# Kernel optimization log

Measured on AMD Instinct MI355X. Metric: run time of the kernel, lower is better.

## Reference

```python
import jax, jax.numpy as jnp
import numpy as np

NEG_SLOPE = 0.2
LN_EPS = 1e-5
NUM_LAYERS = 4
H = 3            # num heads (both modalities)
C_MOL = 512      # molecule channels (in == out, required by the cat in forward)
C_PROT = 1280    # protein channels
VOCAB = 512 * 9 + 1
G_MOL = 512      # molecule graphs
G_PROT = 32      # protein graphs


def _with_self_loops(src, dst, n):
    loop = jnp.arange(n, dtype=src.dtype)
    return jnp.concatenate([src, loop]), jnp.concatenate([dst, loop])


def gat_conv(x, src, dst, W, a_src, a_dst, bias):
    """PyG GATConv, concat=False (head-mean), add_self_loops=True.
    x: [N, Fin], W: [Fin, H*C], a_src/a_dst: [H, C], bias: [C]."""
    n = x.shape[0]
    h = (x @ W).reshape(n, a_src.shape[0], a_src.shape[1])   # [N,H,C]
    al_s = jnp.sum(h * a_src, axis=-1)                       # [N,H]
    al_d = jnp.sum(h * a_dst, axis=-1)                       # [N,H]
    s, d = _with_self_loops(src, dst, n)
    e = jax.nn.leaky_relu(al_s[s] + al_d[d], NEG_SLOPE)      # [E+N,H]
    m = jax.ops.segment_max(e, d, num_segments=n)            # segment softmax (stable)
    m = jnp.where(jnp.isfinite(m), m, 0.0)
    p = jnp.exp(e - m[d])
    z = jax.ops.segment_sum(p, d, num_segments=n)
    alpha = p / (z[d] + 1e-16)                               # [E+N,H]
    out = jax.ops.segment_sum(h[s] * alpha[:, :, None], d, num_segments=n)  # [N,H,C]
    return out.mean(axis=1) + bias                           # concat=False -> head mean


def layer_norm(x, g, b):
    mu = x.mean(-1, keepdims=True)
    var = ((x - mu) ** 2).mean(-1, keepdims=True)
    return (x - mu) * jax.lax.rsqrt(var + LN_EPS) * g + b


def mean_pool(x, batch, num_graphs):
    s = jax.ops.segment_sum(x, batch, num_segments=num_graphs)
    cnt = jax.ops.segment_sum(jnp.ones((x.shape[0],), x.dtype), batch, num_segments=num_graphs)
    return s / jnp.maximum(cnt, 1.0)[:, None]


def setup_inputs() -> dict:
    key = jax.random.key(0)
    ks = jax.random.split(key, 20)
    n_mol, e_mol = 40000, 80000
    n_prot, e_prot = 8000, 64000
    drug_x = jax.random.randint(ks[0], (n_mol, 9), 0, VOCAB)
    mol_edge_index = jax.random.randint(ks[1], (2, e_mol), 0, n_mol)
    mol_batch = jnp.sort(jax.random.randint(ks[2], (n_mol,), 0, G_MOL))
    prot_x = jax.random.normal(ks[3], (n_prot, C_PROT), jnp.float32)
    prot_edge_index = jax.random.randint(ks[4], (2, e_prot), 0, n_prot)
    prot_batch = jnp.sort(jax.random.randint(ks[5], (n_prot,), 0, G_PROT))
    sc = 0.02
    emb = (jax.random.normal(ks[6], (VOCAB, C_MOL), jnp.float32) * sc).at[0].set(0.0)  # padding_idx=0
    mol_W = jax.random.normal(ks[7], (NUM_LAYERS, C_MOL, H * C_MOL), jnp.float32) * sc
    mol_asrc = jax.random.normal(ks[8], (NUM_LAYERS, H, C_MOL), jnp.float32) * sc
    mol_adst = jax.random.normal(ks[9], (NUM_LAYERS, H, C_MOL), jnp.float32) * sc
    mol_bias = jnp.zeros((NUM_LAYERS, C_MOL), jnp.float32)
    mol_ln_g = jnp.ones((NUM_LAYERS, C_MOL), jnp.float32)
    mol_ln_b = jnp.zeros((NUM_LAYERS, C_MOL), jnp.float32)
    prot_W = jax.random.normal(ks[10], (NUM_LAYERS, C_PROT, H * C_PROT), jnp.float32) * sc
    prot_asrc = jax.random.normal(ks[11], (NUM_LAYERS, H, C_PROT), jnp.float32) * sc
    prot_adst = jax.random.normal(ks[12], (NUM_LAYERS, H, C_PROT), jnp.float32) * sc
    prot_bias = jnp.zeros((NUM_LAYERS, C_PROT), jnp.float32)
    prot_ln_g = jnp.ones((NUM_LAYERS, C_PROT), jnp.float32)
    prot_ln_b = jnp.zeros((NUM_LAYERS, C_PROT), jnp.float32)
    return dict(drug_x=drug_x, mol_edge_index=mol_edge_index, mol_batch=mol_batch,
                prot_x=prot_x, prot_edge_index=prot_edge_index, prot_batch=prot_batch,
                emb=emb, mol_W=mol_W, mol_asrc=mol_asrc, mol_adst=mol_adst,
                mol_bias=mol_bias, mol_ln_g=mol_ln_g, mol_ln_b=mol_ln_b,
                prot_W=prot_W, prot_asrc=prot_asrc, prot_adst=prot_adst,
                prot_bias=prot_bias, prot_ln_g=prot_ln_g, prot_ln_b=prot_ln_b)


def reference(drug_x, mol_edge_index, mol_batch, prot_x, prot_edge_index, prot_batch,
              emb, mol_W, mol_asrc, mol_adst, mol_bias, mol_ln_g, mol_ln_b,
              prot_W, prot_asrc, prot_adst, prot_bias, prot_ln_g, prot_ln_b):
    # dropout layers are identity (eval mode)
    mol_x = emb[drug_x].mean(axis=-2)                       # [N_mol, C_MOL]
    mol_feats = [mean_pool(mol_x, mol_batch, G_MOL)]
    prot_feats = [mean_pool(prot_x, prot_batch, G_PROT)]
    msrc, mdst = mol_edge_index[0], mol_edge_index[1]
    psrc, pdst = prot_edge_index[0], prot_edge_index[1]
    px = prot_x
    for i in range(NUM_LAYERS):
        mol_x = gat_conv(mol_x, msrc, mdst, mol_W[i], mol_asrc[i], mol_adst[i], mol_bias[i])
        mol_x = layer_norm(mol_x, mol_ln_g[i], mol_ln_b[i])
        px = gat_conv(px, psrc, pdst, prot_W[i], prot_asrc[i], prot_adst[i], prot_bias[i])
        px = layer_norm(px, prot_ln_g[i], prot_ln_b[i])
        mol_feats.append(mean_pool(mol_x, mol_batch, G_MOL))
        prot_feats.append(mean_pool(px, prot_batch, G_PROT))
    return jnp.stack(mol_feats, axis=1), jnp.stack(prot_feats, axis=1)  # [G,5,C] each
```

## Files before the change

### kernel.cpp

```cpp
#include <hip/hip_runtime.h>
#include <cstdint>


constexpr int H_HEADS = 3;
constexpr float NEG_SLOPE = 0.2f;
constexpr float LN_EPS = 1e-5f;
constexpr int N_MOL = 40000, E_MOL = 80000, C_MOL = 512, G_MOL = 512;
constexpr int N_PROT = 8000, E_PROT = 64000, C_PROT = 1280, G_PROT = 32;
constexpr int LAYERS = 4;
constexpr int MPAD_MOL = 40064;
constexpr int MPAD_PROT = 8064;

typedef unsigned short u16;
typedef __attribute__((ext_vector_type(8))) short short8v;
typedef __attribute__((ext_vector_type(4))) unsigned short ushort4v;
typedef __attribute__((ext_vector_type(4))) float f32x4;

__device__ __forceinline__ float bf2f(u16 s) {
    union { unsigned u; float f; } v; v.u = ((unsigned)s) << 16; return v.f;
}
__device__ __forceinline__ u16 f2bf(float f) {
    union { float f; unsigned u; } v; v.f = f;
    return (u16)((v.u + 0x7fffu + ((v.u >> 16) & 1u)) >> 16);
}

__device__ __forceinline__ void g2l16(const void* g, void* l) {
    __builtin_amdgcn_global_load_lds((const __attribute__((address_space(1))) void*)g,
                                     (__attribute__((address_space(3))) void*)l, 16, 0, 0);
}


__global__ void set_int_kernel(int* p, int v, int n) {
    int i = blockIdx.x * blockDim.x + threadIdx.x;
    if (i < n) p[i] = v;
}

__global__ void zero_f32_kernel(float* p, int n) {
    int i = blockIdx.x * blockDim.x + threadIdx.x;
    if (i < n) p[i] = 0.f;
}

__global__ void copy_int_kernel(const int* __restrict__ s, int* __restrict__ d, int n) {
    int i = blockIdx.x * blockDim.x + threadIdx.x;
    if (i < n) d[i] = s[i];
}

__global__ void hist_kernel(const int* __restrict__ keys, int n, int* __restrict__ cnt) {
    int i = blockIdx.x * blockDim.x + threadIdx.x;
    if (i < n) atomicAdd(&cnt[keys[i]], 1);
}

__global__ void scan_kernel(const int* __restrict__ in, int* __restrict__ out, int n) {
    __shared__ int sums[1024];
    const int t = threadIdx.x;
    const int chunk = (n + 1023) / 1024;
    const int start = t * chunk;
    const int end = min(start + chunk, n);
    int s = 0;
    for (int i = start; i < end; ++i) s += in[i];
    sums[t] = s;
    __syncthreads();
    if (t == 0) {
        int acc = 0;
        for (int i = 0; i < 1024; ++i) { int v = sums[i]; sums[i] = acc; acc += v; }
        out[n] = acc;
    }
    __syncthreads();
    int acc = sums[t];
    for (int i = start; i < end; ++i) { out[i] = acc; acc += in[i]; }
}

__global__ void fill_self_kernel(int* __restrict__ pos, int* __restrict__ srcl, int n) {
    int i = blockIdx.x * blockDim.x + threadIdx.x;
    if (i < n) { int slot = atomicAdd(&pos[i], 1); srcl[slot] = i; }
}

__global__ void fill_edge_kernel(const int* __restrict__ src, const int* __restrict__ dst, int e,
                                 int* __restrict__ pos, int* __restrict__ srcl) {
    int i = blockIdx.x * blockDim.x + threadIdx.x;
    if (i < e) { int slot = atomicAdd(&pos[dst[i]], 1); srcl[slot] = src[i]; }
}

__global__ void f32_to_bf16(const float* __restrict__ in, u16* __restrict__ out, int n) {
    int i = blockIdx.x * blockDim.x + threadIdx.x;
    if (i < n) out[i] = f2bf(in[i]);
}


__global__ void embed_mean_kernel(const int* __restrict__ drug_x, const float* __restrict__ emb,
                                  u16* __restrict__ out) {
    const int n = blockIdx.x;
    __shared__ int idx[9];
    if (threadIdx.x < 9) idx[threadIdx.x] = drug_x[n * 9 + threadIdx.x];
    __syncthreads();
    const int c = threadIdx.x;
    float s = 0.f;
#pragma unroll
    for (int t = 0; t < 9; ++t) s += emb[(size_t)idx[t] * C_MOL + c];
    out[(size_t)n * C_MOL + c] = f2bf(s * (1.f / 9.f));
}


__global__ __launch_bounds__(256) void transfold(const float* __restrict__ W, u16* __restrict__ Wt,
                                                 const float* __restrict__ asrc,
                                                 const float* __restrict__ adst,
                                                 float* __restrict__ wsrc, float* __restrict__ wdst,
                                                 int CIN, int COUT, size_t headStride, int ldn) {
    __shared__ float t[32][33];
    __shared__ float rs[8][33], rd[8][33];
    const int h = blockIdx.z;
    const int n0 = blockIdx.x * 32, k0 = blockIdx.y * 32;
    const int tx = threadIdx.x & 31, ty = threadIdx.x >> 5;
#pragma unroll
    for (int q = 0; q < 4; ++q)
        t[ty + q * 8][tx] = W[(size_t)(k0 + ty + q * 8) * (H_HEADS * COUT) + h * COUT + n0 + tx];
    __syncthreads();
#pragma unroll
    for (int q = 0; q < 4; ++q)
        Wt[(size_t)h * headStride + (size_t)(n0 + ty + q * 8) * ldn + k0 + tx] =
            f2bf(t[tx][ty + q * 8]);
    float ps = 0.f, pd = 0.f;
    const float* as = asrc + h * COUT + n0;
    const float* ad = adst + h * COUT + n0;
#pragma unroll
    for (int q = 0; q < 4; ++q) {
        const float w = t[tx][ty + q * 8];
        ps += w * as[ty + q * 8];
        pd += w * ad[ty + q * 8];
    }
    rs[ty][tx] = ps;
    rd[ty][tx] = pd;
    __syncthreads();
    if (ty == 0) {
        float s = 0.f, d = 0.f;
#pragma unroll
        for (int j = 0; j < 8; ++j) { s += rs[j][tx]; d += rd[j][tx]; }
        atomicAdd(&wsrc[h * CIN + k0 + tx], s);
        atomicAdd(&wdst[h * CIN + k0 + tx], d);
    }
}


template <int C>
__global__ void attn_logits(const u16* __restrict__ x, const float* __restrict__ wsrc,
                            const float* __restrict__ wdst, float* __restrict__ als,
                            float* __restrict__ ald) {
    constexpr int PER = C / 64;
    const int n = blockIdx.x, lane = threadIdx.x;
    const u16* xr = x + (size_t)n * C + lane * PER;
    float xv[PER];
#pragma unroll
    for (int i = 0; i < PER; i += 4) {
        const ushort4v v = *(const ushort4v*)(xr + i);
        xv[i] = bf2f(v.x); xv[i + 1] = bf2f(v.y); xv[i + 2] = bf2f(v.z); xv[i + 3] = bf2f(v.w);
    }
    for (int h = 0; h < H_HEADS; ++h) {
        const float* ws = wsrc + h * C + lane * PER;
        const float* wd = wdst + h * C + lane * PER;
        float ss = 0.f, sd = 0.f;
#pragma unroll
        for (int i = 0; i < PER; i += 4) {
            const float4 a = *(const float4*)(ws + i);
            const float4 b = *(const float4*)(wd + i);
            ss += xv[i] * a.x + xv[i + 1] * a.y + xv[i + 2] * a.z + xv[i + 3] * a.w;
            sd += xv[i] * b.x + xv[i + 1] * b.y + xv[i + 2] * b.z + xv[i + 3] * b.w;
        }
        for (int o = 32; o; o >>= 1) { ss += __shfl_down(ss, o); sd += __shfl_down(sd, o); }
        if (lane == 0) { als[n * H_HEADS + h] = ss; ald[n * H_HEADS + h] = sd; }
    }
}


__global__ void alpha_kernel2(const float* __restrict__ als, const float* __restrict__ ald,
                              const int* __restrict__ indptr, const int* __restrict__ srcl,
                              float* __restrict__ alphaw, int n_nodes) {
    const int t = blockIdx.x * blockDim.x + threadIdx.x;
    const int n = t / H_HEADS, h = t - n * H_HEADS;
    if (n >= n_nodes) return;
    const int beg = indptr[n], end = indptr[n + 1];
    const float ad = ald[n * H_HEADS + h];
    float m = -1e30f;
    for (int e = beg; e < end; ++e) {
        float v = als[srcl[e] * H_HEADS + h] + ad;
        v = v >= 0.f ? v : NEG_SLOPE * v;
        m = fmaxf(m, v);
    }
    float z = 0.f;
    for (int e = beg; e < end; ++e) {
        float v = als[srcl[e] * H_HEADS + h] + ad;
        v = v >= 0.f ? v : NEG_SLOPE * v;
        z += __expf(v - m);
    }
    const float zi = 1.f / (z + 1e-16f);
    for (int e = beg; e < end; ++e) {
        float v = als[srcl[e] * H_HEADS + h] + ad;
        v = v >= 0.f ? v : NEG_SLOPE * v;
        alphaw[e * H_HEADS + h] = __expf(v - m) * zi;
    }
}


__global__ __launch_bounds__(256) void aggregate_mol(const u16* __restrict__ x,
                                                     const float* __restrict__ alphaw,
                                                     const int* __restrict__ indptr,
                                                     const int* __restrict__ srcl,
                                                     u16* __restrict__ agg) {
    const int wv = threadIdx.x >> 6, lane = threadIdx.x & 63;
    const int n = blockIdx.x * 4 + wv;
    const int beg = indptr[n], end = indptr[n + 1];
    float acc[H_HEADS][8];
#pragma unroll
    for (int h = 0; h < H_HEADS; ++h)
#pragma unroll
        for (int j = 0; j < 8; ++j) acc[h][j] = 0.f;
    for (int e = beg; e < end; ++e) {
        const float a0 = alphaw[e * H_HEADS + 0];
        const float a1 = alphaw[e * H_HEADS + 1];
        const float a2 = alphaw[e * H_HEADS + 2];
        const short8v row = *(const short8v*)(x + (size_t)srcl[e] * C_MOL + lane * 8);
#pragma unroll
        for (int j = 0; j < 8; ++j) {
            const float f = bf2f((u16)row[j]);
            acc[0][j] += a0 * f; acc[1][j] += a1 * f; acc[2][j] += a2 * f;
        }
    }
    u16* o = agg + (size_t)n * (3 * C_MOL) + lane * 8;
#pragma unroll
    for (int h = 0; h < H_HEADS; ++h) {
        short8v r;
#pragma unroll
        for (int j = 0; j < 8; ++j) r[j] = (short)f2bf(acc[h][j]);
        *(short8v*)(o + h * C_MOL) = r;
    }
}


template <int C>
__global__ void aggregate_all3(const u16* __restrict__ x, const float* __restrict__ alphaw,
                               const int* __restrict__ indptr, const int* __restrict__ srcl,
                               u16* __restrict__ agg) {
    const int n = blockIdx.x, tid = threadIdx.x;
    const int beg = indptr[n], end = indptr[n + 1];
    float acc[H_HEADS][4];
#pragma unroll
    for (int h = 0; h < H_HEADS; ++h)
#pragma unroll
        for (int j = 0; j < 4; ++j) acc[h][j] = 0.f;
    for (int e = beg; e < end; ++e) {
        const float a0 = alphaw[e * H_HEADS + 0];
        const float a1 = alphaw[e * H_HEADS + 1];
        const float a2 = alphaw[e * H_HEADS + 2];
        const ushort4v v = *(const ushort4v*)(x + (size_t)srcl[e] * C + tid * 4);
        const float f0 = bf2f(v.x), f1 = bf2f(v.y), f2 = bf2f(v.z), f3 = bf2f(v.w);
        acc[0][0] += a0 * f0; acc[0][1] += a0 * f1; acc[0][2] += a0 * f2; acc[0][3] += a0 * f3;
        acc[1][0] += a1 * f0; acc[1][1] += a1 * f1; acc[1][2] += a1 * f2; acc[1][3] += a1 * f3;
        acc[2][0] += a2 * f0; acc[2][1] += a2 * f1; acc[2][2] += a2 * f2; acc[2][3] += a2 * f3;
    }
    u16* o = agg + (size_t)n * (3 * C) + tid * 4;
#pragma unroll
    for (int h = 0; h < H_HEADS; ++h) {
        ushort4v r;
        r.x = f2bf(acc[h][0]); r.y = f2bf(acc[h][1]); r.z = f2bf(acc[h][2]); r.w = f2bf(acc[h][3]);
        *(ushort4v*)(o + h * C) = r;
    }
}


__global__ __launch_bounds__(512) void gemm_dual(
    const u16* __restrict__ A0, const u16* __restrict__ B0, u16* __restrict__ C0,
    int N0, int K0, int nx0, int M0, int g0,
    const u16* __restrict__ A1, const u16* __restrict__ B1, u16* __restrict__ C1,
    int N1, int K1, int nx1, int M1) {
    __shared__ u16 lds[49152];
    const int tid = threadIdx.x;
    const int w = tid >> 6, l = tid & 63;
    const int wr = w >> 2, wc = w & 3;

    const int bid = blockIdx.x;
    const u16 *A, *Bt;
    u16* Cout;
    int N, K, nxch, Mreal, base, sz;
    if (bid < g0) { base = 0; sz = g0; A = A0; Bt = B0; Cout = C0; N = N0; K = K0; nxch = nx0; Mreal = M0; }
    else { base = g0; sz = gridDim.x - g0; A = A1; Bt = B1; Cout = C1; N = N1; K = K1; nxch = nx1; Mreal = M1; }
    const int j = bid - base;
    const int q = sz >> 3, r = sz & 7;
    const int xcd = j & 7, idx = j >> 3;
    const int wg = (xcd < r ? xcd * (q + 1) : r * (q + 1) + (xcd - r) * q) + idx;
    const int nx = wg % nxch, my = wg / nxch;
    const size_t bm = (size_t)my * 128, bn = (size_t)nx * 256;

    const f32x4 zf = {0.f, 0.f, 0.f, 0.f};
    f32x4 acc[4][4];
#pragma unroll
    for (int i = 0; i < 4; ++i)
#pragma unroll
        for (int jj = 0; jj < 4; ++jj) acc[i][jj] = zf;

    const int sseg = (l & 7) ^ (l >> 3);
    const u16* Ab = A + (bm + w * 16 + (l >> 3)) * (size_t)K + sseg * 8;
    const u16* Bb = Bt + (bn + w * 32 + (l >> 3)) * (size_t)K + sseg * 8;

    auto stage = [&](int buf, int k0) {
        u16* La = lds + buf * 24576;
#pragma unroll
        for (int qq = 0; qq < 2; ++qq)
            g2l16(Ab + k0 + (size_t)qq * 8 * K, La + (w * 2 + qq) * 512);
#pragma unroll
        for (int qq = 0; qq < 4; ++qq)
            g2l16(Bb + k0 + (size_t)qq * 8 * K, La + 8192 + (w * 4 + qq) * 512);
    };

    const int nt = K >> 6;
    stage(0, 0);
    for (int t = 0; t < nt; ++t) {
        const int cur = t & 1;
        if (t + 1 < nt) {
            stage(cur ^ 1, (t + 1) << 6);
            asm volatile("s_waitcnt vmcnt(6)" ::: "memory");
        } else {
            asm volatile("s_waitcnt vmcnt(0)" ::: "memory");
        }
        __builtin_amdgcn_s_barrier();
        __builtin_amdgcn_sched_barrier(0);
        const u16* Lb = lds + cur * 24576;
#pragma unroll
        for (int kk = 0; kk < 2; ++kk) {
            const int gs = kk * 4 + (l >> 4);
            const int sg = (gs ^ (l & 7)) * 8;
            short8v af[4], bf8[4];
#pragma unroll
            for (int fm = 0; fm < 4; ++fm) {
                const int row = wr * 64 + fm * 16 + (l & 15);
                af[fm] = *(const short8v*)&Lb[row * 64 + sg];
            }
#pragma unroll
            for (int fn = 0; fn < 4; ++fn) {
                const int row = wc * 64 + fn * 16 + (l & 15);
                bf8[fn] = *(const short8v*)&Lb[8192 + row * 64 + sg];
            }
#pragma unroll
            for (int fm = 0; fm < 4; ++fm)
#pragma unroll
                for (int fn = 0; fn < 4; ++fn)
                    acc[fm][fn] = __builtin_amdgcn_mfma_f32_16x16x32_bf16(af[fm], bf8[fn],
                                                                          acc[fm][fn], 0, 0, 0);
        }
        __builtin_amdgcn_sched_barrier(0);
        __builtin_amdgcn_s_barrier();
    }

#pragma unroll
    for (int half = 0; half < 2; ++half) {
        if (wr == half) {
#pragma unroll
            for (int fm = 0; fm < 4; ++fm)
#pragma unroll
                for (int fn = 0; fn < 4; ++fn) {
                    const int col = wc * 64 + fn * 16 + (l & 15);
#pragma unroll
                    for (int rr = 0; rr < 4; ++rr)
                        lds[(fm * 16 + (l >> 4) * 4 + rr) * 264 + col] = f2bf(acc[fm][fn][rr]);
                }
        }
        __syncthreads();
        const int lrow = tid >> 3, lseg = tid & 7;
        const size_t grow = bm + half * 64 + lrow;
        if (grow < (size_t)Mreal) {
            u16* Crow = Cout + grow * (size_t)N + bn + lseg * 32;
            const u16* Lr = lds + lrow * 264 + lseg * 32;
#pragma unroll
            for (int ii = 0; ii < 4; ++ii)
                *(float4*)(Crow + ii * 8) = *(const float4*)(Lr + ii * 8);
        }
        __syncthreads();
    }
}


template <int C, int LOGITS>
__global__ __launch_bounds__(256) void ln_kernel(u16* __restrict__ x,
                                                 const float* __restrict__ bias,
                                                 const float* __restrict__ g,
                                                 const float* __restrict__ b,
                                                 const float* __restrict__ wsrc_n,
                                                 const float* __restrict__ wdst_n,
                                                 float* __restrict__ als, float* __restrict__ ald) {
    constexpr int PER = C / 256;
    const int n = blockIdx.x, tid = threadIdx.x;
    u16* xr = x + (size_t)n * C;
    float vals[PER];
    float s1 = 0.f, s2 = 0.f;
    constexpr float invH = 1.f / (float)H_HEADS;
#pragma unroll
    for (int i = 0; i < PER; ++i) {
        const int c = i * 256 + tid;
        const float v = bf2f(xr[c]) * invH + bias[c];
        vals[i] = v;
        s1 += v;
        s2 += v * v;
    }
    __shared__ float red[2][4];
    __shared__ float red2[4][6];
    for (int o = 32; o; o >>= 1) { s1 += __shfl_down(s1, o); s2 += __shfl_down(s2, o); }
    if ((tid & 63) == 0) { red[0][tid >> 6] = s1; red[1][tid >> 6] = s2; }
    __syncthreads();
    const float t1 = red[0][0] + red[0][1] + red[0][2] + red[0][3];
    const float t2 = red[1][0] + red[1][1] + red[1][2] + red[1][3];
    const float mu = t1 / C;
    const float var = t2 / C - mu * mu;
    const float rstd = rsqrtf(var + LN_EPS);
    float ps0 = 0.f, ps1 = 0.f, ps2 = 0.f, pd0 = 0.f, pd1 = 0.f, pd2 = 0.f;
#pragma unroll
    for (int i = 0; i < PER; ++i) {
        const int c = i * 256 + tid;
        const u16 xq16 = f2bf((vals[i] - mu) * rstd * g[c] + b[c]);
        xr[c] = xq16;
        if (LOGITS) {
            const float xq = bf2f(xq16);
            ps0 += xq * wsrc_n[0 * C + c]; pd0 += xq * wdst_n[0 * C + c];
            ps1 += xq * wsrc_n[1 * C + c]; pd1 += xq * wdst_n[1 * C + c];
            ps2 += xq * wsrc_n[2 * C + c]; pd2 += xq * wdst_n[2 * C + c];
        }
    }
    if (LOGITS) {
        for (int o = 32; o; o >>= 1) {
            ps0 += __shfl_down(ps0, o); ps1 += __shfl_down(ps1, o); ps2 += __shfl_down(ps2, o);
            pd0 += __shfl_down(pd0, o); pd1 += __shfl_down(pd1, o); pd2 += __shfl_down(pd2, o);
        }
        __syncthreads();
        if ((tid & 63) == 0) {
            const int wv = tid >> 6;
            red2[wv][0] = ps0; red2[wv][1] = ps1; red2[wv][2] = ps2;
            red2[wv][3] = pd0; red2[wv][4] = pd1; red2[wv][5] = pd2;
        }
        __syncthreads();
        if (tid == 0) {
#pragma unroll
            for (int h = 0; h < H_HEADS; ++h) {
                als[n * H_HEADS + h] = red2[0][h] + red2[1][h] + red2[2][h] + red2[3][h];
                ald[n * H_HEADS + h] =
                    red2[0][3 + h] + red2[1][3 + h] + red2[2][3 + h] + red2[3][3 + h];
            }
        }
    }
}


template <int C, int S>
__global__ void pool_atomic(const u16* __restrict__ x, const int* __restrict__ goff,
                            float* __restrict__ out, int layer) {
    const int g = blockIdx.x, seg = blockIdx.y;
    const int beg = goff[g], end = goff[g + 1];
    const int len = end - beg;
    const int s0 = beg + (len * seg) / S;
    const int s1 = beg + (len * (seg + 1)) / S;
    if (s0 >= s1) return;
    const float inv = 1.f / fmaxf((float)len, 1.f);
    const int tid = threadIdx.x;
    float a0 = 0.f, a1 = 0.f, a2 = 0.f, a3 = 0.f;
    for (int n = s0; n < s1; ++n) {
        const ushort4v v = *(const ushort4v*)(x + (size_t)n * C + tid * 4);
        a0 += bf2f(v.x); a1 += bf2f(v.y); a2 += bf2f(v.z); a3 += bf2f(v.w);
    }
    float* o = out + ((size_t)g * (LAYERS + 1) + layer) * C + tid * 4;
    atomicAdd(o + 0, a0 * inv);
    atomicAdd(o + 1, a1 * inv);
    atomicAdd(o + 2, a2 * inv);
    atomicAdd(o + 3, a3 * inv);
}


extern "C" void kernel_launch(void* const* d_in, const int* in_sizes, int n_in, void* d_out,
                              int out_size, void* d_ws, size_t ws_size, hipStream_t stream) {
    const int* drug_x      = (const int*)d_in[0];
    const int* mol_ei      = (const int*)d_in[1];
    const int* mol_batch   = (const int*)d_in[2];
    const float* prot_in   = (const float*)d_in[3];
    const int* prot_ei     = (const int*)d_in[4];
    const int* prot_batch  = (const int*)d_in[5];
    const float* emb       = (const float*)d_in[6];
    const float* mol_W     = (const float*)d_in[7];
    const float* mol_asrc  = (const float*)d_in[8];
    const float* mol_adst  = (const float*)d_in[9];
    const float* mol_bias  = (const float*)d_in[10];
    const float* mol_lng   = (const float*)d_in[11];
    const float* mol_lnb   = (const float*)d_in[12];
    const float* prot_W    = (const float*)d_in[13];
    const float* prot_asrc = (const float*)d_in[14];
    const float* prot_adst = (const float*)d_in[15];
    const float* prot_bias = (const float*)d_in[16];
    const float* prot_lng  = (const float*)d_in[17];
    const float* prot_lnb  = (const float*)d_in[18];

    if (ws_size < (size_t)240500000) return;
    const bool BIG = ws_size >= (size_t)262000000;

    char* base = (char*)d_ws;
    size_t off = 0;
    auto alloc = [&](size_t bytes) -> void* {
        void* r = base + off;
        off = (off + bytes + 255) & ~(size_t)255;
        return r;
    };
    u16* x_mol  = (u16*)alloc((size_t)N_MOL * C_MOL * 2);
    u16* x_prot = (u16*)alloc((size_t)N_PROT * C_PROT * 2);
    u16* aggM   = (u16*)alloc((size_t)3 * MPAD_MOL * C_MOL * 2);
    u16* WtM    = (u16*)alloc((size_t)H_HEADS * C_MOL * C_MOL * 2);
    u16* WtP    = (u16*)alloc((size_t)H_HEADS * C_PROT * C_PROT * 2);
    u16* aggP   = BIG ? (u16*)alloc((size_t)3 * MPAD_PROT * C_PROT * 2) : aggM;
    float* wsrcM = (float*)alloc((size_t)LAYERS * H_HEADS * C_MOL * 4);
    float* wdstM = (float*)alloc((size_t)LAYERS * H_HEADS * C_MOL * 4);
    float* wsrcP = (float*)alloc((size_t)LAYERS * H_HEADS * C_PROT * 4);
    float* wdstP = (float*)alloc((size_t)LAYERS * H_HEADS * C_PROT * 4);
    float* alsM = (float*)alloc((size_t)N_MOL * H_HEADS * 4);
    float* aldM = (float*)alloc((size_t)N_MOL * H_HEADS * 4);
    float* alsP = (float*)alloc((size_t)N_PROT * H_HEADS * 4);
    float* aldP = (float*)alloc((size_t)N_PROT * H_HEADS * 4);
    float* alphaw = (float*)alloc((size_t)(E_MOL + N_MOL) * H_HEADS * 4);
    int* mol_indptr  = (int*)alloc((N_MOL + 1) * 4);
    int* mol_pos     = (int*)alloc(N_MOL * 4);
    int* mol_srcl    = (int*)alloc((E_MOL + N_MOL) * 4);
    int* prot_indptr = (int*)alloc((N_PROT + 1) * 4);
    int* prot_pos    = (int*)alloc(N_PROT * 4);
    int* prot_srcl   = (int*)alloc((E_PROT + N_PROT) * 4);
    int* cnt         = (int*)alloc(N_MOL * 4);
    int* mol_goff    = (int*)alloc((G_MOL + 1) * 4);
    int* prot_goff   = (int*)alloc((G_PROT + 1) * 4);
    int* gcnt        = (int*)alloc(G_MOL * 4);

    float* out_mol  = (float*)d_out;
    float* out_prot = (float*)d_out + (size_t)G_MOL * (LAYERS + 1) * C_MOL;

    zero_f32_kernel<<<(out_size + 255) / 256, 256, 0, stream>>>((float*)d_out, out_size);
    zero_f32_kernel<<<(LAYERS * H_HEADS * C_MOL + 255) / 256, 256, 0, stream>>>(
        wsrcM, LAYERS * H_HEADS * C_MOL);
    zero_f32_kernel<<<(LAYERS * H_HEADS * C_MOL + 255) / 256, 256, 0, stream>>>(
        wdstM, LAYERS * H_HEADS * C_MOL);
    zero_f32_kernel<<<(LAYERS * H_HEADS * C_PROT + 255) / 256, 256, 0, stream>>>(
        wsrcP, LAYERS * H_HEADS * C_PROT);
    zero_f32_kernel<<<(LAYERS * H_HEADS * C_PROT + 255) / 256, 256, 0, stream>>>(
        wdstP, LAYERS * H_HEADS * C_PROT);

    set_int_kernel<<<(N_MOL + 255) / 256, 256, 0, stream>>>(cnt, 1, N_MOL);
    hist_kernel<<<(E_MOL + 255) / 256, 256, 0, stream>>>(mol_ei + E_MOL, E_MOL, cnt);
    scan_kernel<<<1, 1024, 0, stream>>>(cnt, mol_indptr, N_MOL);
    copy_int_kernel<<<(N_MOL + 255) / 256, 256, 0, stream>>>(mol_indptr, mol_pos, N_MOL);
    fill_self_kernel<<<(N_MOL + 255) / 256, 256, 0, stream>>>(mol_pos, mol_srcl, N_MOL);
    fill_edge_kernel<<<(E_MOL + 255) / 256, 256, 0, stream>>>(mol_ei, mol_ei + E_MOL, E_MOL, mol_pos,
                                                              mol_srcl);
    set_int_kernel<<<(N_PROT + 255) / 256, 256, 0, stream>>>(cnt, 1, N_PROT);
    hist_kernel<<<(E_PROT + 255) / 256, 256, 0, stream>>>(prot_ei + E_PROT, E_PROT, cnt);
    scan_kernel<<<1, 1024, 0, stream>>>(cnt, prot_indptr, N_PROT);
    copy_int_kernel<<<(N_PROT + 255) / 256, 256, 0, stream>>>(prot_indptr, prot_pos, N_PROT);
    fill_self_kernel<<<(N_PROT + 255) / 256, 256, 0, stream>>>(prot_pos, prot_srcl, N_PROT);
    fill_edge_kernel<<<(E_PROT + 255) / 256, 256, 0, stream>>>(prot_ei, prot_ei + E_PROT, E_PROT,
                                                               prot_pos, prot_srcl);

    set_int_kernel<<<(G_MOL + 255) / 256, 256, 0, stream>>>(gcnt, 0, G_MOL);
    hist_kernel<<<(N_MOL + 255) / 256, 256, 0, stream>>>(mol_batch, N_MOL, gcnt);
    scan_kernel<<<1, 1024, 0, stream>>>(gcnt, mol_goff, G_MOL);
    set_int_kernel<<<(G_PROT + 255) / 256, 256, 0, stream>>>(gcnt, 0, G_PROT);
    hist_kernel<<<(N_PROT + 255) / 256, 256, 0, stream>>>(prot_batch, N_PROT, gcnt);
    scan_kernel<<<1, 1024, 0, stream>>>(gcnt, prot_goff, G_PROT);

    transfold<<<dim3(C_MOL / 32, C_MOL / 32, H_HEADS), 256, 0, stream>>>(
        mol_W, WtM, mol_asrc, mol_adst, wsrcM, wdstM, C_MOL, C_MOL, (size_t)C_MOL, 3 * C_MOL);
    transfold<<<dim3(C_PROT / 32, C_PROT / 32, H_HEADS), 256, 0, stream>>>(
        prot_W, WtP, prot_asrc, prot_adst, wsrcP, wdstP, C_PROT, C_PROT, (size_t)C_PROT,
        3 * C_PROT);

    f32_to_bf16<<<(N_PROT * C_PROT + 255) / 256, 256, 0, stream>>>(prot_in, x_prot, N_PROT * C_PROT);
    embed_mean_kernel<<<N_MOL, C_MOL, 0, stream>>>(drug_x, emb, x_mol);
    pool_atomic<C_MOL, 8><<<dim3(G_MOL, 8), C_MOL / 4, 0, stream>>>(x_mol, mol_goff, out_mol, 0);
    pool_atomic<C_PROT, 64><<<dim3(G_PROT, 64), C_PROT / 4, 0, stream>>>(x_prot, prot_goff,
                                                                         out_prot, 0);
    attn_logits<C_MOL><<<N_MOL, 64, 0, stream>>>(x_mol, wsrcM, wdstM, alsM, aldM);
    attn_logits<C_PROT><<<N_PROT, 64, 0, stream>>>(x_prot, wsrcP, wdstP, alsP, aldP);

    const int gMol = (C_MOL / 256) * (MPAD_MOL / 128);
    const int gProt = (C_PROT / 256) * (MPAD_PROT / 128);

    for (int l = 0; l < LAYERS; ++l) {
        const int last = (l == LAYERS - 1);
        if (BIG) {
            alpha_kernel2<<<(N_MOL * H_HEADS + 255) / 256, 256, 0, stream>>>(
                alsM, aldM, mol_indptr, mol_srcl, alphaw, N_MOL);
            aggregate_mol<<<N_MOL / 4, 256, 0, stream>>>(x_mol, alphaw, mol_indptr, mol_srcl, aggM);
            alpha_kernel2<<<(N_PROT * H_HEADS + 255) / 256, 256, 0, stream>>>(
                alsP, aldP, prot_indptr, prot_srcl, alphaw, N_PROT);
            aggregate_all3<C_PROT><<<N_PROT, C_PROT / 4, 0, stream>>>(x_prot, alphaw, prot_indptr,
                                                                      prot_srcl, aggP);
            gemm_dual<<<gProt + gMol, 512, 0, stream>>>(
                aggP, WtP, x_prot, C_PROT, 3 * C_PROT, C_PROT / 256, N_PROT, gProt,
                aggM, WtM, x_mol, C_MOL, 3 * C_MOL, C_MOL / 256, N_MOL);
            if (!last) {
                transfold<<<dim3(C_MOL / 32, C_MOL / 32, H_HEADS), 256, 0, stream>>>(
                    mol_W + (size_t)(l + 1) * C_MOL * (H_HEADS * C_MOL), WtM,
                    mol_asrc + (size_t)(l + 1) * H_HEADS * C_MOL,
                    mol_adst + (size_t)(l + 1) * H_HEADS * C_MOL,
                    wsrcM + (size_t)(l + 1) * H_HEADS * C_MOL,
                    wdstM + (size_t)(l + 1) * H_HEADS * C_MOL, C_MOL, C_MOL, (size_t)C_MOL,
                    3 * C_MOL);
                transfold<<<dim3(C_PROT / 32, C_PROT / 32, H_HEADS), 256, 0, stream>>>(
                    prot_W + (size_t)(l + 1) * C_PROT * (H_HEADS * C_PROT), WtP,
                    prot_asrc + (size_t)(l + 1) * H_HEADS * C_PROT,
                    prot_adst + (size_t)(l + 1) * H_HEADS * C_PROT,
                    wsrcP + (size_t)(l + 1) * H_HEADS * C_PROT,
                    wdstP + (size_t)(l + 1) * H_HEADS * C_PROT, C_PROT, C_PROT, (size_t)C_PROT,
                    3 * C_PROT);
                ln_kernel<C_MOL, 1><<<N_MOL, 256, 0, stream>>>(
                    x_mol, mol_bias + (size_t)l * C_MOL, mol_lng + (size_t)l * C_MOL,
                    mol_lnb + (size_t)l * C_MOL, wsrcM + (size_t)(l + 1) * H_HEADS * C_MOL,
                    wdstM + (size_t)(l + 1) * H_HEADS * C_MOL, alsM, aldM);
                ln_kernel<C_PROT, 1><<<N_PROT, 256, 0, stream>>>(
                    x_prot, prot_bias + (size_t)l * C_PROT, prot_lng + (size_t)l * C_PROT,
                    prot_lnb + (size_t)l * C_PROT, wsrcP + (size_t)(l + 1) * H_HEADS * C_PROT,
                    wdstP + (size_t)(l + 1) * H_HEADS * C_PROT, alsP, aldP);
            } else {
                ln_kernel<C_MOL, 0><<<N_MOL, 256, 0, stream>>>(
                    x_mol, mol_bias + (size_t)l * C_MOL, mol_lng + (size_t)l * C_MOL,
                    mol_lnb + (size_t)l * C_MOL, nullptr, nullptr, nullptr, nullptr);
                ln_kernel<C_PROT, 0><<<N_PROT, 256, 0, stream>>>(
                    x_prot, prot_bias + (size_t)l * C_PROT, prot_lng + (size_t)l * C_PROT,
                    prot_lnb + (size_t)l * C_PROT, nullptr, nullptr, nullptr, nullptr);
            }
            pool_atomic<C_MOL, 8><<<dim3(G_MOL, 8), C_MOL / 4, 0, stream>>>(x_mol, mol_goff,
                                                                            out_mol, l + 1);
            pool_atomic<C_PROT, 64><<<dim3(G_PROT, 64), C_PROT / 4, 0, stream>>>(
                x_prot, prot_goff, out_prot, l + 1);
        } else {
            alpha_kernel2<<<(N_MOL * H_HEADS + 255) / 256, 256, 0, stream>>>(
                alsM, aldM, mol_indptr, mol_srcl, alphaw, N_MOL);
            aggregate_mol<<<N_MOL / 4, 256, 0, stream>>>(x_mol, alphaw, mol_indptr, mol_srcl, aggM);
            gemm_dual<<<gMol, 512, 0, stream>>>(
                aggM, WtM, x_mol, C_MOL, 3 * C_MOL, C_MOL / 256, N_MOL, gMol,
                aggM, WtM, x_mol, C_MOL, 3 * C_MOL, C_MOL / 256, N_MOL);
            if (!last)
                transfold<<<dim3(C_MOL / 32, C_MOL / 32, H_HEADS), 256, 0, stream>>>(
                    mol_W + (size_t)(l + 1) * C_MOL * (H_HEADS * C_MOL), WtM,
                    mol_asrc + (size_t)(l + 1) * H_HEADS * C_MOL,
                    mol_adst + (size_t)(l + 1) * H_HEADS * C_MOL,
                    wsrcM + (size_t)(l + 1) * H_HEADS * C_MOL,
                    wdstM + (size_t)(l + 1) * H_HEADS * C_MOL, C_MOL, C_MOL, (size_t)C_MOL,
                    3 * C_MOL);
            if (last)
                ln_kernel<C_MOL, 0><<<N_MOL, 256, 0, stream>>>(
                    x_mol, mol_bias + (size_t)l * C_MOL, mol_lng + (size_t)l * C_MOL,
                    mol_lnb + (size_t)l * C_MOL, nullptr, nullptr, nullptr, nullptr);
            else
                ln_kernel<C_MOL, 1><<<N_MOL, 256, 0, stream>>>(
                    x_mol, mol_bias + (size_t)l * C_MOL, mol_lng + (size_t)l * C_MOL,
                    mol_lnb + (size_t)l * C_MOL, wsrcM + (size_t)(l + 1) * H_HEADS * C_MOL,
                    wdstM + (size_t)(l + 1) * H_HEADS * C_MOL, alsM, aldM);
            pool_atomic<C_MOL, 8><<<dim3(G_MOL, 8), C_MOL / 4, 0, stream>>>(x_mol, mol_goff,
                                                                            out_mol, l + 1);
            alpha_kernel2<<<(N_PROT * H_HEADS + 255) / 256, 256, 0, stream>>>(
                alsP, aldP, prot_indptr, prot_srcl, alphaw, N_PROT);
            aggregate_all3<C_PROT><<<N_PROT, C_PROT / 4, 0, stream>>>(x_prot, alphaw, prot_indptr,
                                                                      prot_srcl, aggP);
            gemm_dual<<<gProt, 512, 0, stream>>>(
                aggP, WtP, x_prot, C_PROT, 3 * C_PROT, C_PROT / 256, N_PROT, gProt,
                aggP, WtP, x_prot, C_PROT, 3 * C_PROT, C_PROT / 256, N_PROT);
            if (!last)
                transfold<<<dim3(C_PROT / 32, C_PROT / 32, H_HEADS), 256, 0, stream>>>(
                    prot_W + (size_t)(l + 1) * C_PROT * (H_HEADS * C_PROT), WtP,
                    prot_asrc + (size_t)(l + 1) * H_HEADS * C_PROT,
                    prot_adst + (size_t)(l + 1) * H_HEADS * C_PROT,
                    wsrcP + (size_t)(l + 1) * H_HEADS * C_PROT,
                    wdstP + (size_t)(l + 1) * H_HEADS * C_PROT, C_PROT, C_PROT, (size_t)C_PROT,
                    3 * C_PROT);
            if (last)
                ln_kernel<C_PROT, 0><<<N_PROT, 256, 0, stream>>>(
                    x_prot, prot_bias + (size_t)l * C_PROT, prot_lng + (size_t)l * C_PROT,
                    prot_lnb + (size_t)l * C_PROT, nullptr, nullptr, nullptr, nullptr);
            else
                ln_kernel<C_PROT, 1><<<N_PROT, 256, 0, stream>>>(
                    x_prot, prot_bias + (size_t)l * C_PROT, prot_lng + (size_t)l * C_PROT,
                    prot_lnb + (size_t)l * C_PROT, wsrcP + (size_t)(l + 1) * H_HEADS * C_PROT,
                    wdstP + (size_t)(l + 1) * H_HEADS * C_PROT, alsP, aldP);
            pool_atomic<C_PROT, 64><<<dim3(G_PROT, 64), C_PROT / 4, 0, stream>>>(
                x_prot, prot_goff, out_prot, l + 1);
        }
    }
}
```

Measured before the change: 2.344 ms.

## Replace 128x256 double-buffered GEMM with single-buffered 128x128 tile kernel

Replaces the 512-thread, 128x256-tile, double-buffered LDS GEMM with a 256-thread 128x128-tile kernel that uses one LDS buffer and plain __syncthreads between load and compute. The grid doubles in workgroup count and LDS use per block drops sharply, so more blocks fit per CU and the smaller channel dimensions tile more evenly. The cost is losing the explicit overlap of global-to-LDS loads with MFMA work, and reloading A once for each additional N tile.

```diff
diff --git a/kernel.cpp b/kernel.cpp
--- a/kernel.cpp
+++ b/kernel.cpp
@@ -266,15 +266,15 @@
 }
 
 
-__global__ __launch_bounds__(512) void gemm_dual(
+__global__ __launch_bounds__(256) void gemm128d(
     const u16* __restrict__ A0, const u16* __restrict__ B0, u16* __restrict__ C0,
     int N0, int K0, int nx0, int M0, int g0,
     const u16* __restrict__ A1, const u16* __restrict__ B1, u16* __restrict__ C1,
     int N1, int K1, int nx1, int M1) {
-    __shared__ u16 lds[49152];
+    __shared__ u16 lds[16384];
     const int tid = threadIdx.x;
     const int w = tid >> 6, l = tid & 63;
-    const int wr = w >> 2, wc = w & 3;
+    const int wr = w >> 1, wc = w & 1;
 
     const int bid = blockIdx.x;
     const u16 *A, *Bt;
@@ -287,7 +287,7 @@
     const int xcd = j & 7, idx = j >> 3;
     const int wg = (xcd < r ? xcd * (q + 1) : r * (q + 1) + (xcd - r) * q) + idx;
     const int nx = wg % nxch, my = wg / nxch;
-    const size_t bm = (size_t)my * 128, bn = (size_t)nx * 256;
+    const size_t bm = (size_t)my * 128, bn = (size_t)nx * 128;
 
     const f32x4 zf = {0.f, 0.f, 0.f, 0.f};
     f32x4 acc[4][4];
@@ -296,47 +296,32 @@
 #pragma unroll
         for (int jj = 0; jj < 4; ++jj) acc[i][jj] = zf;
 
+    const int srow = w * 32 + (l >> 3);
     const int sseg = (l & 7) ^ (l >> 3);
-    const u16* Ab = A + (bm + w * 16 + (l >> 3)) * (size_t)K + sseg * 8;
-    const u16* Bb = Bt + (bn + w * 32 + (l >> 3)) * (size_t)K + sseg * 8;
-
-    auto stage = [&](int buf, int k0) {
-        u16* La = lds + buf * 24576;
-#pragma unroll
-        for (int qq = 0; qq < 2; ++qq)
-            g2l16(Ab + k0 + (size_t)qq * 8 * K, La + (w * 2 + qq) * 512);
+    const u16* Ab = A + (bm + srow) * (size_t)K + sseg * 8;
+    const u16* Bb = Bt + (bn + srow) * (size_t)K + sseg * 8;
+
+    for (int k0 = 0; k0 < K; k0 += 64) {
 #pragma unroll
         for (int qq = 0; qq < 4; ++qq)
-            g2l16(Bb + k0 + (size_t)qq * 8 * K, La + 8192 + (w * 4 + qq) * 512);
-    };
-
-    const int nt = K >> 6;
-    stage(0, 0);
-    for (int t = 0; t < nt; ++t) {
-        const int cur = t & 1;
-        if (t + 1 < nt) {
-            stage(cur ^ 1, (t + 1) << 6);
-            asm volatile("s_waitcnt vmcnt(6)" ::: "memory");
-        } else {
-            asm volatile("s_waitcnt vmcnt(0)" ::: "memory");
-        }
-        __builtin_amdgcn_s_barrier();
-        __builtin_amdgcn_sched_barrier(0);
-        const u16* Lb = lds + cur * 24576;
+            g2l16(Ab + k0 + (size_t)qq * 8 * K, lds + (w * 4 + qq) * 512);
+#pragma unroll
+        for (int qq = 0; qq < 4; ++qq)
+            g2l16(Bb + k0 + (size_t)qq * 8 * K, lds + 8192 + (w * 4 + qq) * 512);
+        __syncthreads();
 #pragma unroll
         for (int kk = 0; kk < 2; ++kk) {
-            const int gs = kk * 4 + (l >> 4);
-            const int sg = (gs ^ (l & 7)) * 8;
+            const int sg = ((kk * 4 + (l >> 4)) ^ (l & 7)) * 8;
             short8v af[4], bf8[4];
 #pragma unroll
             for (int fm = 0; fm < 4; ++fm) {
                 const int row = wr * 64 + fm * 16 + (l & 15);
-                af[fm] = *(const short8v*)&Lb[row * 64 + sg];
+                af[fm] = *(const short8v*)&lds[row * 64 + sg];
             }
 #pragma unroll
             for (int fn = 0; fn < 4; ++fn) {
                 const int row = wc * 64 + fn * 16 + (l & 15);
-                bf8[fn] = *(const short8v*)&Lb[8192 + row * 64 + sg];
+                bf8[fn] = *(const short8v*)&lds[8192 + row * 64 + sg];
             }
 #pragma unroll
             for (int fm = 0; fm < 4; ++fm)
@@ -345,8 +330,7 @@
                     acc[fm][fn] = __builtin_amdgcn_mfma_f32_16x16x32_bf16(af[fm], bf8[fn],
                                                                           acc[fm][fn], 0, 0, 0);
         }
-        __builtin_amdgcn_sched_barrier(0);
-        __builtin_amdgcn_s_barrier();
+        __syncthreads();
     }
 
 #pragma unroll
@@ -359,15 +343,15 @@
                     const int col = wc * 64 + fn * 16 + (l & 15);
 #pragma unroll
                     for (int rr = 0; rr < 4; ++rr)
-                        lds[(fm * 16 + (l >> 4) * 4 + rr) * 264 + col] = f2bf(acc[fm][fn][rr]);
+                        lds[(fm * 16 + (l >> 4) * 4 + rr) * 136 + col] = f2bf(acc[fm][fn][rr]);
                 }
         }
         __syncthreads();
-        const int lrow = tid >> 3, lseg = tid & 7;
+        const int lrow = tid >> 2, lseg = tid & 3;
         const size_t grow = bm + half * 64 + lrow;
         if (grow < (size_t)Mreal) {
             u16* Crow = Cout + grow * (size_t)N + bn + lseg * 32;
-            const u16* Lr = lds + lrow * 264 + lseg * 32;
+            const u16* Lr = lds + lrow * 136 + lseg * 32;
 #pragma unroll
             for (int ii = 0; ii < 4; ++ii)
                 *(float4*)(Crow + ii * 8) = *(const float4*)(Lr + ii * 8);
@@ -577,8 +561,8 @@
     attn_logits<C_MOL><<<N_MOL, 64, 0, stream>>>(x_mol, wsrcM, wdstM, alsM, aldM);
     attn_logits<C_PROT><<<N_PROT, 64, 0, stream>>>(x_prot, wsrcP, wdstP, alsP, aldP);
 
-    const int gMol = (C_MOL / 256) * (MPAD_MOL / 128);
-    const int gProt = (C_PROT / 256) * (MPAD_PROT / 128);
+    const int gMol = (MPAD_MOL / 128) * (C_MOL / 128);
+    const int gProt = (MPAD_PROT / 128) * (C_PROT / 128);
 
     for (int l = 0; l < LAYERS; ++l) {
         const int last = (l == LAYERS - 1);
@@ -590,9 +574,9 @@
                 alsP, aldP, prot_indptr, prot_srcl, alphaw, N_PROT);
             aggregate_all3<C_PROT><<<N_PROT, C_PROT / 4, 0, stream>>>(x_prot, alphaw, prot_indptr,
                                                                       prot_srcl, aggP);
-            gemm_dual<<<gProt + gMol, 512, 0, stream>>>(
-                aggP, WtP, x_prot, C_PROT, 3 * C_PROT, C_PROT / 256, N_PROT, gProt,
-                aggM, WtM, x_mol, C_MOL, 3 * C_MOL, C_MOL / 256, N_MOL);
+            gemm128d<<<gProt + gMol, 256, 0, stream>>>(
+                aggP, WtP, x_prot, C_PROT, 3 * C_PROT, C_PROT / 128, N_PROT, gProt,
+                aggM, WtM, x_mol, C_MOL, 3 * C_MOL, C_MOL / 128, N_MOL);
             if (!last) {
                 transfold<<<dim3(C_MOL / 32, C_MOL / 32, H_HEADS), 256, 0, stream>>>(
                     mol_W + (size_t)(l + 1) * C_MOL * (H_HEADS * C_MOL), WtM,
@@ -632,9 +616,9 @@
             alpha_kernel2<<<(N_MOL * H_HEADS + 255) / 256, 256, 0, stream>>>(
                 alsM, aldM, mol_indptr, mol_srcl, alphaw, N_MOL);
             aggregate_mol<<<N_MOL / 4, 256, 0, stream>>>(x_mol, alphaw, mol_indptr, mol_srcl, aggM);
-            gemm_dual<<<gMol, 512, 0, stream>>>(
-                aggM, WtM, x_mol, C_MOL, 3 * C_MOL, C_MOL / 256, N_MOL, gMol,
-                aggM, WtM, x_mol, C_MOL, 3 * C_MOL, C_MOL / 256, N_MOL);
+            gemm128d<<<gMol, 256, 0, stream>>>(
+                aggM, WtM, x_mol, C_MOL, 3 * C_MOL, C_MOL / 128, N_MOL, gMol,
+                aggM, WtM, x_mol, C_MOL, 3 * C_MOL, C_MOL / 128, N_MOL);
             if (!last)
                 transfold<<<dim3(C_MOL / 32, C_MOL / 32, H_HEADS), 256, 0, stream>>>(
                     mol_W + (size_t)(l + 1) * C_MOL * (H_HEADS * C_MOL), WtM,
@@ -658,9 +642,9 @@
                 alsP, aldP, prot_indptr, prot_srcl, alphaw, N_PROT);
             aggregate_all3<C_PROT><<<N_PROT, C_PROT / 4, 0, stream>>>(x_prot, alphaw, prot_indptr,
                                                                       prot_srcl, aggP);
-            gemm_dual<<<gProt, 512, 0, stream>>>(
-                aggP, WtP, x_prot, C_PROT, 3 * C_PROT, C_PROT / 256, N_PROT, gProt,
-                aggP, WtP, x_prot, C_PROT, 3 * C_PROT, C_PROT / 256, N_PROT);
+            gemm128d<<<gProt, 256, 0, stream>>>(
+                aggP, WtP, x_prot, C_PROT, 3 * C_PROT, C_PROT / 128, N_PROT, gProt,
+                aggP, WtP, x_prot, C_PROT, 3 * C_PROT, C_PROT / 128, N_PROT);
             if (!last)
                 transfold<<<dim3(C_PROT / 32, C_PROT / 32, H_HEADS), 256, 0, stream>>>(
                     prot_W + (size_t)(l + 1) * C_PROT * (H_HEADS * C_PROT), WtP,
```

Measured after the change: 2.290 ms. 1.02x faster.
